# Performance work log

Measured on AMD Instinct MI355X. Metric: run time of the kernel, lower is better.

The kernel has to match this reference:

```python
import jax, jax.numpy as jnp
import numpy as np
from jax import lax

B, T, F, D, K = 64, 1000, 140, 256, 7
TAU, V_TH, EPS, ALPHA = 2.0, 1.0, 1e-5, 2.0
PAD = (K - 1) // 2

# Heaviside spike with ATan surrogate gradient (spikingjelly default, alpha=2)
@jax.custom_vjp
def spike_fn(x):
    return (x >= 0.0).astype(x.dtype)

def _spike_fwd(x):
    return spike_fn(x), x

def _spike_bwd(x, g):
    sg = (ALPHA / 2.0) / (1.0 + (jnp.pi / 2.0 * ALPHA * x) ** 2)
    return (g * sg,)

spike_fn.defvjp(_spike_fwd, _spike_bwd)

def lif(x_seq):
    """Multi-step LIF: v += (x - v)/tau, hard reset to 0 on spike. x_seq: (T,B,D)."""
    def step(v, x):
        v = v + (x - v) / TAU
        s = spike_fn(v - V_TH)
        return v * (1.0 - s), s
    _, spikes = lax.scan(step, jnp.zeros_like(x_seq[0]), x_seq)
    return spikes

def bn(x, g, b, m, v):
    # eval-mode BatchNorm1d over channel dim D (last axis of (T,B,D))
    return (x - m) * (g * lax.rsqrt(v + EPS)) + b

def setup_inputs() -> dict:
    key = jax.random.key(0)
    ks = jax.random.split(key, 4)
    s = 0.05
    return {
        "x": jax.random.normal(ks[0], (B, T, F), jnp.float32),
        "pw_w": jax.random.normal(ks[1], (D, F), jnp.float32) * s,
        "pw_b": jnp.zeros((D,), jnp.float32),
        "dw_w": jax.random.normal(ks[2], (D, 1, K), jnp.float32) * s,  # depthwise (O,I/g,K)
        "bn1_g": jnp.ones((D,), jnp.float32),
        "bn1_b": jnp.zeros((D,), jnp.float32),
        "bn1_m": jnp.zeros((D,), jnp.float32),
        "bn1_v": jnp.ones((D,), jnp.float32),
        "lin_w": jax.random.normal(ks[3], (D, D), jnp.float32) * s,
        "bn2_g": jnp.ones((D,), jnp.float32),
        "bn2_b": jnp.zeros((D,), jnp.float32),
        "bn2_m": jnp.zeros((D,), jnp.float32),
        "bn2_v": jnp.ones((D,), jnp.float32),
    }

def reference(x, pw_w, pw_b, dw_w, bn1_g, bn1_b, bn1_m, bn1_v,
              lin_w, bn2_g, bn2_b, bn2_m, bn2_v):
    # pointwise conv: (B,T,F) -> (B,D,T)
    h = jnp.einsum('btf,df->bdt', x, pw_w) + pw_b[None, :, None]
    # depthwise temporal conv, groups=D, same padding
    h = lax.conv_general_dilated(h, dw_w, window_strides=(1,),
                                 padding=[(PAD, PAD)], feature_group_count=D,
                                 dimension_numbers=('NCH', 'OIH', 'NCH'))
    h = jnp.transpose(h, (2, 0, 1))  # (T,B,D) multi-step layout
    h = lif(bn(h, bn1_g, bn1_b, bn1_m, bn1_v))
    residual = h
    h = jnp.einsum('tbd,ed->tbe', h, lin_w)
    h = lif(bn(h, bn2_g, bn2_b, bn2_m, bn2_v))
    return h + residual
```

## Files before the change

### kernel.cpp

```cpp
#include <hip/hip_runtime.h>
#include <hip/hip_bf16.h>

#define B_  64
#define T_  1000
#define F_  140
#define D_  256
#define EPS_ 1e-5f

#define CL_ 50
#define NC_ 20
#define W_  24

#define CW2_ 96
#define NCH_ 11
#define HST_ 132

typedef __attribute__((ext_vector_type(8))) short bf16x8;
typedef __attribute__((ext_vector_type(4))) float f32x4;
typedef unsigned long long u64;

static __device__ inline short f2bf(float f) {
  __hip_bfloat16 h = __float2bfloat16(f);
  return *reinterpret_cast<short*>(&h);
}
static __device__ inline float bf2f(short s) {
  unsigned int u = ((unsigned int)(unsigned short)s) << 16;
  return __uint_as_float(u);
}

__global__ __launch_bounds__(256) void k0_prep(const float* __restrict__ lw,
                                               float* __restrict__ lwT,
                                               const float* __restrict__ pw,
                                               short* __restrict__ wbf) {
  int i = blockIdx.x * 256 + threadIdx.x;
  if (i < 65536) {
    int e = i >> 8, d = i & 255;
    lwT[(size_t)d * D_ + e] = lw[(size_t)e * D_ + d];
  } else if (i < 65536 + 256 * 160) {
    int j = i - 65536;
    int n = j / 160, k = j - n * 160;
    wbf[j] = (k < F_) ? f2bf(pw[(size_t)n * F_ + k]) : (short)0;
  }
}

__global__ __launch_bounds__(256) void k12_fused(const float* __restrict__ x,
                                                 const short* __restrict__ wbf,
                                                 const float* __restrict__ bias,
                                                 const float* __restrict__ dww,
                                                 const float* __restrict__ g1,
                                                 const float* __restrict__ b1,
                                                 const float* __restrict__ m1,
                                                 const float* __restrict__ v1,
                                                 u64* __restrict__ bits) {
  __shared__ short smem[20480];
  short* As = smem;
  short* Bs = smem + 10240;
  const int b = blockIdx.x;
  const int c = blockIdx.y;
  const int half = blockIdx.z;
  const int n0g = half * 128;
  const int tb = CW2_ * c - 27;
  const int tid = threadIdx.x;
  const int lane = tid & 63, wv = tid >> 6;
  const int lr = lane & 15, quad = lane >> 4;
  const int mr = (wv & 1) * 64, nc0 = (wv >> 1) * 64;

  const int srow = tid >> 1;
  const int kh = (tid & 1) * 16;
  const int ta = tb + srow;
  const bool arow_ok = (ta >= 0) && (ta < T_);
  const float* xrow = x + ((size_t)b * T_ + ta) * F_;
  const short* wrow = wbf + (size_t)(n0g + srow) * 160 + kh;

  auto stage = [&](int kc, int buf) {
    short tmp[16];
#pragma unroll
    for (int q = 0; q < 4; q++) {
      int kg = kc + kh + q * 4;
      float4 av = make_float4(0.f, 0.f, 0.f, 0.f);
      if (arow_ok && kg < F_) av = *(const float4*)(xrow + kg);
      tmp[q * 4 + 0] = f2bf(av.x); tmp[q * 4 + 1] = f2bf(av.y);
      tmp[q * 4 + 2] = f2bf(av.z); tmp[q * 4 + 3] = f2bf(av.w);
    }
    short* ap = As + buf * 5120 + srow * 40 + kh;
    *(bf16x8*)(ap + 0) = *(bf16x8*)(tmp + 0);
    *(bf16x8*)(ap + 8) = *(bf16x8*)(tmp + 8);
    short* bp = Bs + buf * 5120 + srow * 40 + kh;
    *(bf16x8*)(bp + 0) = *(const bf16x8*)(wrow + kc + 0);
    *(bf16x8*)(bp + 8) = *(const bf16x8*)(wrow + kc + 8);
  };

  f32x4 acc[4][4] = {};
  stage(0, 0);
  __syncthreads();
#pragma unroll
  for (int kk = 0; kk < 5; kk++) {
    const int cur = kk & 1;
    if (kk < 4) stage((kk + 1) * 32, cur ^ 1);
    const short* ap = As + cur * 5120 + quad * 8;
    const short* bp = Bs + cur * 5120 + quad * 8;
    bf16x8 af[4], bfr[4];
#pragma unroll
    for (int i = 0; i < 4; i++) af[i] = *(const bf16x8*)(ap + (mr + i * 16 + lr) * 40);
#pragma unroll
    for (int j = 0; j < 4; j++) bfr[j] = *(const bf16x8*)(bp + (nc0 + j * 16 + lr) * 40);
#pragma unroll
    for (int i = 0; i < 4; i++)
#pragma unroll
      for (int j = 0; j < 4; j++)
        acc[i][j] = __builtin_amdgcn_mfma_f32_16x16x32_bf16(af[i], bfr[j], acc[i][j], 0, 0, 0);
    __syncthreads();
  }

  short* hbuf = smem;
#pragma unroll
  for (int j = 0; j < 4; j++) {
    const int n = nc0 + j * 16 + lr;
    const float badd = bias[n0g + n];
#pragma unroll
    for (int i = 0; i < 4; i++) {
      const int m = mr + i * 16 + quad * 4;
#pragma unroll
      for (int r = 0; r < 4; r++) {
        const int t = tb + m + r;
        short val = (t >= 0 && t < T_) ? f2bf(acc[i][j][r] + badd) : (short)0;
        hbuf[(m + r) * HST_ + n] = val;
      }
    }
  }
  __syncthreads();

  if (tid < 128) {
    const int d = n0g + tid;
    const float scv = g1[d] * rsqrtf(v1[d] + EPS_);
    float w2[7];
#pragma unroll
    for (int k = 0; k < 7; k++) w2[k] = dww[d * 7 + k] * (0.5f * scv);
    const float sh2 = 0.5f * (b1[d] - m1[d] * scv);

    const int wb = (c == 0) ? 24 : 0;
    float win0 = bf2f(hbuf[(wb + 0) * HST_ + tid]);
    float win1 = bf2f(hbuf[(wb + 1) * HST_ + tid]);
    float win2 = bf2f(hbuf[(wb + 2) * HST_ + tid]);
    float win3 = bf2f(hbuf[(wb + 3) * HST_ + tid]);
    float win4 = bf2f(hbuf[(wb + 4) * HST_ + tid]);
    float win5 = bf2f(hbuf[(wb + 5) * HST_ + tid]);
    float v = 0.f;

    if (c != 0) {
#pragma unroll
      for (int s0 = 0; s0 < 24; s0 += 8) {
        float tap[8];
#pragma unroll
        for (int g = 0; g < 8; g++) tap[g] = bf2f(hbuf[(s0 + g + 6) * HST_ + tid]);
#pragma unroll
        for (int g = 0; g < 8; g++) {
          float u2 = win0 * w2[0] + win1 * w2[1] + win2 * w2[2] + win3 * w2[3] +
                     win4 * w2[4] + win5 * w2[5] + tap[g] * w2[6] + sh2;
          v = 0.5f * v + u2;
          v = (v >= 1.0f) ? 0.f : v;
          win0 = win1; win1 = win2; win2 = win3; win3 = win4; win4 = win5; win5 = tap[g];
        }
      }
    }
    const int tw0 = CW2_ * c;
    const int dq = half * 2 + (tid >> 6);
    u64* bp2 = bits + ((size_t)b * T_ + tw0) * 4 + dq;
    const bool lane0 = ((tid & 63) == 0);
    const int smax = T_ - tw0;
#pragma unroll
    for (int s0 = 0; s0 < 96; s0 += 8) {
      float tap[8];
#pragma unroll
      for (int g = 0; g < 8; g++) tap[g] = bf2f(hbuf[(s0 + g + 30) * HST_ + tid]);
#pragma unroll
      for (int g = 0; g < 8; g++) {
        float u2 = win0 * w2[0] + win1 * w2[1] + win2 * w2[2] + win3 * w2[3] +
                   win4 * w2[4] + win5 * w2[5] + tap[g] * w2[6] + sh2;
        v = 0.5f * v + u2;
        bool sp = (v >= 1.0f);
        u64 mask = __ballot(sp);
        if (lane0 && (s0 + g) < smax) bp2[(size_t)(s0 + g) * 4] = mask;
        v = sp ? 0.f : v;
        win0 = win1; win1 = win2; win2 = win3; win3 = win4; win4 = win5; win5 = tap[g];
      }
    }
  }
}

__global__ __launch_bounds__(256) void k3_lin_lif(const u64* __restrict__ bits,
                                                  const float* __restrict__ lwT,
                                                  const float* __restrict__ g2,
                                                  const float* __restrict__ b2,
                                                  const float* __restrict__ m2,
                                                  const float* __restrict__ v2,
                                                  float* __restrict__ out) {
  __shared__ u64 sb[(CL_ + W_) * 4];
  const int b = blockIdx.x;
  const int t0 = blockIdx.y * CL_;
  const int tstart = (t0 >= W_) ? t0 - W_ : 0;
  const int nwarm = t0 - tstart;
  const int nsteps = nwarm + CL_;
  const int e = threadIdx.x;
  const u64* gbp = bits + ((size_t)b * T_ + tstart) * 4;
  for (int i = e; i < nsteps * 4; i += 256) sb[i] = gbp[i];
  __syncthreads();

  const float sc = g2[e] * rsqrtf(v2[e] + EPS_);
  const float shf = b2[e] - m2[e] * sc;
  const int eq = e >> 6, eb = e & 63;
  float v = 0.f;

  if (nwarm) {
#pragma unroll
    for (int s0 = 0; s0 < 24; s0 += 4) {
      u64 a0[4], a1[4], a2[4], a3[4];
#pragma unroll
      for (int g = 0; g < 4; g++) {
        a0[g] = sb[(s0 + g) * 4 + 0]; a1[g] = sb[(s0 + g) * 4 + 1];
        a2[g] = sb[(s0 + g) * 4 + 2]; a3[g] = sb[(s0 + g) * 4 + 3];
      }
#pragma unroll
      for (int g = 0; g < 4; g++) {
        float u = shf;
        if (a0[g] | a1[g] | a2[g] | a3[g]) {
          float acc = 0.f;
          u64 mm;
          mm = a0[g]; while (mm) { int l = __builtin_ctzll(mm); mm &= mm - 1; acc += lwT[(size_t)(l) * D_ + e]; }
          mm = a1[g]; while (mm) { int l = __builtin_ctzll(mm); mm &= mm - 1; acc += lwT[(size_t)(64 + l) * D_ + e]; }
          mm = a2[g]; while (mm) { int l = __builtin_ctzll(mm); mm &= mm - 1; acc += lwT[(size_t)(128 + l) * D_ + e]; }
          mm = a3[g]; while (mm) { int l = __builtin_ctzll(mm); mm &= mm - 1; acc += lwT[(size_t)(192 + l) * D_ + e]; }
          u = acc * sc + shf;
        }
        v = 0.5f * (v + u);
        v = (v >= 1.0f) ? 0.f : v;
      }
    }
  }
  float* op = out + ((size_t)t0 * B_ + b) * D_ + e;
  const size_t ts = (size_t)B_ * D_;
#pragma unroll
  for (int s0 = 0; s0 < 50; s0 += 5) {
    u64 a0[5], a1[5], a2[5], a3[5];
#pragma unroll
    for (int g = 0; g < 5; g++) {
      const int s = nwarm + s0 + g;
      a0[g] = sb[s * 4 + 0]; a1[g] = sb[s * 4 + 1];
      a2[g] = sb[s * 4 + 2]; a3[g] = sb[s * 4 + 3];
    }
#pragma unroll
    for (int g = 0; g < 5; g++) {
      float u = shf;
      if (a0[g] | a1[g] | a2[g] | a3[g]) {
        float acc = 0.f;
        u64 mm;
        mm = a0[g]; while (mm) { int l = __builtin_ctzll(mm); mm &= mm - 1; acc += lwT[(size_t)(l) * D_ + e]; }
        mm = a1[g]; while (mm) { int l = __builtin_ctzll(mm); mm &= mm - 1; acc += lwT[(size_t)(64 + l) * D_ + e]; }
        mm = a2[g]; while (mm) { int l = __builtin_ctzll(mm); mm &= mm - 1; acc += lwT[(size_t)(128 + l) * D_ + e]; }
        mm = a3[g]; while (mm) { int l = __builtin_ctzll(mm); mm &= mm - 1; acc += lwT[(size_t)(192 + l) * D_ + e]; }
        u = acc * sc + shf;
      }
      v = 0.5f * (v + u);
      bool sp = (v >= 1.0f);
      u64 myw = (eq == 0) ? a0[g] : (eq == 1) ? a1[g] : (eq == 2) ? a2[g] : a3[g];
      float s1 = (float)((myw >> eb) & 1ull);
      op[(size_t)(s0 + g) * ts] = (sp ? 1.0f : 0.0f) + s1;
      v = sp ? 0.f : v;
    }
  }
}

extern "C" void kernel_launch(void* const* d_in, const int* in_sizes, int n_in,
                              void* d_out, int out_size, void* d_ws, size_t ws_size,
                              hipStream_t stream) {
  const float* x    = (const float*)d_in[0];
  const float* pw_w = (const float*)d_in[1];
  const float* pw_b = (const float*)d_in[2];
  const float* dw_w = (const float*)d_in[3];
  const float* g1   = (const float*)d_in[4];
  const float* b1   = (const float*)d_in[5];
  const float* m1   = (const float*)d_in[6];
  const float* v1   = (const float*)d_in[7];
  const float* lw   = (const float*)d_in[8];
  const float* g2   = (const float*)d_in[9];
  const float* b2   = (const float*)d_in[10];
  const float* m2   = (const float*)d_in[11];
  const float* v2   = (const float*)d_in[12];
  float* out = (float*)d_out;

  char* ws = (char*)d_ws;
  u64* bits = (u64*)ws;
  float* lwT = (float*)(ws + 2048000);
  short* wbf = (short*)(ws + 2048000 + 262144);

  k0_prep<<<(65536 + 256 * 160 + 255) / 256, 256, 0, stream>>>(lw, lwT, pw_w, wbf);
  dim3 g_k12(B_, NCH_, 2);
  k12_fused<<<g_k12, 256, 0, stream>>>(x, wbf, pw_b, dw_w, g1, b1, m1, v1, bits);
  dim3 g_k3(B_, NC_);
  k3_lin_lif<<<g_k3, 256, 0, stream>>>(bits, lwT, g2, b2, m2, v2, out);
}
```

Baseline: 176.9 us.

## Restructure fused conv-LIF kernel into short 34-step chunks covering all channels

The fused pointwise-conv plus depthwise-conv plus LIF kernel now gives each block all 256 channels and a 34-step time window instead of half the channels over 96 steps. This makes the grid 64x30 rather than 64x11x2, so all 256 threads take part in the serial LIF scan and each thread's sequential chain is shorter. The pointwise weights are pre-swizzled into MFMA fragment order and loaded straight from global memory, and the whole A tile is staged once instead of double-buffered. In exchange, the 27-step warm-up recompute is a much larger share of each chunk, and the larger LDS footprint may lower occupancy.

```diff
diff --git a/kernel.cpp b/kernel.cpp
--- a/kernel.cpp
+++ b/kernel.cpp
@@ -11,11 +11,13 @@
 #define NC_ 20
 #define W_  24
 
-#define CW2_ 96
-#define NCH_ 11
-#define HST_ 132
+#define CW3_ 34
+#define NCH3_ 30
+#define HST3_ 268
+#define AST_ 168
 
 typedef __attribute__((ext_vector_type(8))) short bf16x8;
+typedef __attribute__((ext_vector_type(4))) short bf16x4;
 typedef __attribute__((ext_vector_type(4))) float f32x4;
 typedef unsigned long long u64;
 
@@ -31,20 +33,25 @@
 __global__ __launch_bounds__(256) void k0_prep(const float* __restrict__ lw,
                                                float* __restrict__ lwT,
                                                const float* __restrict__ pw,
-                                               short* __restrict__ wbf) {
+                                               short* __restrict__ wfrag) {
   int i = blockIdx.x * 256 + threadIdx.x;
   if (i < 65536) {
     int e = i >> 8, d = i & 255;
     lwT[(size_t)d * D_ + e] = lw[(size_t)e * D_ + d];
-  } else if (i < 65536 + 256 * 160) {
+  } else if (i < 65536 + 40960) {
     int j = i - 65536;
-    int n = j / 160, k = j - n * 160;
-    wbf[j] = (k < F_) ? f2bf(pw[(size_t)n * F_ + k]) : (short)0;
+    int q = j & 7;
+    int lane = (j >> 3) & 63;
+    int rest = j >> 9;
+    int kk = rest % 5, ntile = rest / 5;
+    int n = ntile * 16 + (lane & 15);
+    int k = kk * 32 + (lane >> 4) * 8 + q;
+    wfrag[j] = (k < F_) ? f2bf(pw[(size_t)n * F_ + k]) : (short)0;
   }
 }
 
 __global__ __launch_bounds__(256) void k12_fused(const float* __restrict__ x,
-                                                 const short* __restrict__ wbf,
+                                                 const short* __restrict__ wfrag,
                                                  const float* __restrict__ bias,
                                                  const float* __restrict__ dww,
                                                  const float* __restrict__ g1,
@@ -52,86 +59,84 @@
                                                  const float* __restrict__ m1,
                                                  const float* __restrict__ v1,
                                                  u64* __restrict__ bits) {
-  __shared__ short smem[20480];
-  short* As = smem;
-  short* Bs = smem + 10240;
+  __shared__ short smem[64 * HST3_];
+  short* Abuf = smem;
+  short* hbuf = smem;
   const int b = blockIdx.x;
   const int c = blockIdx.y;
-  const int half = blockIdx.z;
-  const int n0g = half * 128;
-  const int tb = CW2_ * c - 27;
+  const int tb = CW3_ * c - 27;
   const int tid = threadIdx.x;
   const int lane = tid & 63, wv = tid >> 6;
   const int lr = lane & 15, quad = lane >> 4;
-  const int mr = (wv & 1) * 64, nc0 = (wv >> 1) * 64;
-
-  const int srow = tid >> 1;
-  const int kh = (tid & 1) * 16;
-  const int ta = tb + srow;
-  const bool arow_ok = (ta >= 0) && (ta < T_);
-  const float* xrow = x + ((size_t)b * T_ + ta) * F_;
-  const short* wrow = wbf + (size_t)(n0g + srow) * 160 + kh;
-
-  auto stage = [&](int kc, int buf) {
-    short tmp[16];
-#pragma unroll
-    for (int q = 0; q < 4; q++) {
-      int kg = kc + kh + q * 4;
-      float4 av = make_float4(0.f, 0.f, 0.f, 0.f);
-      if (arow_ok && kg < F_) av = *(const float4*)(xrow + kg);
-      tmp[q * 4 + 0] = f2bf(av.x); tmp[q * 4 + 1] = f2bf(av.y);
-      tmp[q * 4 + 2] = f2bf(av.z); tmp[q * 4 + 3] = f2bf(av.w);
-    }
-    short* ap = As + buf * 5120 + srow * 40 + kh;
-    *(bf16x8*)(ap + 0) = *(bf16x8*)(tmp + 0);
-    *(bf16x8*)(ap + 8) = *(bf16x8*)(tmp + 8);
-    short* bp = Bs + buf * 5120 + srow * 40 + kh;
-    *(bf16x8*)(bp + 0) = *(const bf16x8*)(wrow + kc + 0);
-    *(bf16x8*)(bp + 8) = *(const bf16x8*)(wrow + kc + 8);
-  };
+
+  {
+    const int arow = tid >> 2, aseg = tid & 3;
+    const int ak0 = aseg * 36;
+    const int anum4 = (aseg == 3) ? 8 : 9;
+    const int ta = tb + arow;
+    short* adst = Abuf + arow * AST_ + ak0;
+    if (ta >= 0 && ta < T_) {
+      const float* xrow = x + ((size_t)b * T_ + ta) * F_ + ak0;
+#pragma unroll
+      for (int q = 0; q < 9; q++) {
+        if (q < anum4) {
+          float4 av = *(const float4*)(xrow + q * 4);
+          bf16x4 pk = {f2bf(av.x), f2bf(av.y), f2bf(av.z), f2bf(av.w)};
+          *(bf16x4*)(adst + q * 4) = pk;
+        }
+      }
+    } else {
+      bf16x4 z = {0, 0, 0, 0};
+#pragma unroll
+      for (int q = 0; q < 9; q++)
+        if (q < anum4) *(bf16x4*)(adst + q * 4) = z;
+    }
+    if (aseg == 3) {
+      bf16x4 z = {0, 0, 0, 0};
+#pragma unroll
+      for (int q = 0; q < 5; q++) *(bf16x4*)(adst + 32 + q * 4) = z;
+    }
+  }
+  __syncthreads();
 
   f32x4 acc[4][4] = {};
-  stage(0, 0);
-  __syncthreads();
+  const short* wfb = wfrag + (size_t)(wv * 4 * 5) * 512 + lane * 8;
 #pragma unroll
   for (int kk = 0; kk < 5; kk++) {
-    const int cur = kk & 1;
-    if (kk < 4) stage((kk + 1) * 32, cur ^ 1);
-    const short* ap = As + cur * 5120 + quad * 8;
-    const short* bp = Bs + cur * 5120 + quad * 8;
-    bf16x8 af[4], bfr[4];
-#pragma unroll
-    for (int i = 0; i < 4; i++) af[i] = *(const bf16x8*)(ap + (mr + i * 16 + lr) * 40);
-#pragma unroll
-    for (int j = 0; j < 4; j++) bfr[j] = *(const bf16x8*)(bp + (nc0 + j * 16 + lr) * 40);
+    bf16x8 bfr[4], af[4];
+#pragma unroll
+    for (int j = 0; j < 4; j++)
+      bfr[j] = *(const bf16x8*)(wfb + (size_t)(j * 5 + kk) * 512);
+#pragma unroll
+    for (int i = 0; i < 4; i++)
+      af[i] = *(const bf16x8*)(Abuf + (i * 16 + lr) * AST_ + kk * 32 + quad * 8);
 #pragma unroll
     for (int i = 0; i < 4; i++)
 #pragma unroll
       for (int j = 0; j < 4; j++)
         acc[i][j] = __builtin_amdgcn_mfma_f32_16x16x32_bf16(af[i], bfr[j], acc[i][j], 0, 0, 0);
-    __syncthreads();
-  }
-
-  short* hbuf = smem;
+  }
+  __syncthreads();
+
 #pragma unroll
   for (int j = 0; j < 4; j++) {
-    const int n = nc0 + j * 16 + lr;
-    const float badd = bias[n0g + n];
+    const int n = wv * 64 + j * 16 + lr;
+    const float badd = bias[n];
 #pragma unroll
     for (int i = 0; i < 4; i++) {
-      const int m = mr + i * 16 + quad * 4;
 #pragma unroll
       for (int r = 0; r < 4; r++) {
-        const int t = tb + m + r;
+        const int row = i * 16 + quad * 4 + r;
+        const int t = tb + row;
         short val = (t >= 0 && t < T_) ? f2bf(acc[i][j][r] + badd) : (short)0;
-        hbuf[(m + r) * HST_ + n] = val;
+        hbuf[row * HST3_ + n] = val;
       }
     }
   }
   __syncthreads();
 
-  if (tid < 128) {
-    const int d = n0g + tid;
+  {
+    const int d = tid;
     const float scv = g1[d] * rsqrtf(v1[d] + EPS_);
     float w2[7];
 #pragma unroll
@@ -139,12 +144,12 @@
     const float sh2 = 0.5f * (b1[d] - m1[d] * scv);
 
     const int wb = (c == 0) ? 24 : 0;
-    float win0 = bf2f(hbuf[(wb + 0) * HST_ + tid]);
-    float win1 = bf2f(hbuf[(wb + 1) * HST_ + tid]);
-    float win2 = bf2f(hbuf[(wb + 2) * HST_ + tid]);
-    float win3 = bf2f(hbuf[(wb + 3) * HST_ + tid]);
-    float win4 = bf2f(hbuf[(wb + 4) * HST_ + tid]);
-    float win5 = bf2f(hbuf[(wb + 5) * HST_ + tid]);
+    float win0 = bf2f(hbuf[(wb + 0) * HST3_ + d]);
+    float win1 = bf2f(hbuf[(wb + 1) * HST3_ + d]);
+    float win2 = bf2f(hbuf[(wb + 2) * HST3_ + d]);
+    float win3 = bf2f(hbuf[(wb + 3) * HST3_ + d]);
+    float win4 = bf2f(hbuf[(wb + 4) * HST3_ + d]);
+    float win5 = bf2f(hbuf[(wb + 5) * HST3_ + d]);
     float v = 0.f;
 
     if (c != 0) {
@@ -152,7 +157,7 @@
       for (int s0 = 0; s0 < 24; s0 += 8) {
         float tap[8];
 #pragma unroll
-        for (int g = 0; g < 8; g++) tap[g] = bf2f(hbuf[(s0 + g + 6) * HST_ + tid]);
+        for (int g = 0; g < 8; g++) tap[g] = bf2f(hbuf[(s0 + g + 6) * HST3_ + d]);
 #pragma unroll
         for (int g = 0; g < 8; g++) {
           float u2 = win0 * w2[0] + win1 * w2[1] + win2 * w2[2] + win3 * w2[3] +
@@ -163,16 +168,15 @@
         }
       }
     }
-    const int tw0 = CW2_ * c;
-    const int dq = half * 2 + (tid >> 6);
-    u64* bp2 = bits + ((size_t)b * T_ + tw0) * 4 + dq;
-    const bool lane0 = ((tid & 63) == 0);
+    const int tw0 = CW3_ * c;
     const int smax = T_ - tw0;
-#pragma unroll
-    for (int s0 = 0; s0 < 96; s0 += 8) {
+    u64* bp = bits + ((size_t)b * T_ + tw0) * 4 + wv;
+    const bool lane0 = (lane == 0);
+#pragma unroll
+    for (int s0 = 0; s0 < 32; s0 += 8) {
       float tap[8];
 #pragma unroll
-      for (int g = 0; g < 8; g++) tap[g] = bf2f(hbuf[(s0 + g + 30) * HST_ + tid]);
+      for (int g = 0; g < 8; g++) tap[g] = bf2f(hbuf[(s0 + g + 30) * HST3_ + d]);
 #pragma unroll
       for (int g = 0; g < 8; g++) {
         float u2 = win0 * w2[0] + win1 * w2[1] + win2 * w2[2] + win3 * w2[3] +
@@ -180,7 +184,23 @@
         v = 0.5f * v + u2;
         bool sp = (v >= 1.0f);
         u64 mask = __ballot(sp);
-        if (lane0 && (s0 + g) < smax) bp2[(size_t)(s0 + g) * 4] = mask;
+        if (lane0 && (s0 + g) < smax) bp[(size_t)(s0 + g) * 4] = mask;
+        v = sp ? 0.f : v;
+        win0 = win1; win1 = win2; win2 = win3; win3 = win4; win4 = win5; win5 = tap[g];
+      }
+    }
+    {
+      float tap[2];
+#pragma unroll
+      for (int g = 0; g < 2; g++) tap[g] = bf2f(hbuf[(32 + g + 30) * HST3_ + d]);
+#pragma unroll
+      for (int g = 0; g < 2; g++) {
+        float u2 = win0 * w2[0] + win1 * w2[1] + win2 * w2[2] + win3 * w2[3] +
+                   win4 * w2[4] + win5 * w2[5] + tap[g] * w2[6] + sh2;
+        v = 0.5f * v + u2;
+        bool sp = (v >= 1.0f);
+        u64 mask = __ballot(sp);
+        if (lane0 && (32 + g) < smax) bp[(size_t)(32 + g) * 4] = mask;
         v = sp ? 0.f : v;
         win0 = win1; win1 = win2; win2 = win3; win3 = win4; win4 = win5; win5 = tap[g];
       }
@@ -291,11 +311,11 @@
   char* ws = (char*)d_ws;
   u64* bits = (u64*)ws;
   float* lwT = (float*)(ws + 2048000);
-  short* wbf = (short*)(ws + 2048000 + 262144);
-
-  k0_prep<<<(65536 + 256 * 160 + 255) / 256, 256, 0, stream>>>(lw, lwT, pw_w, wbf);
-  dim3 g_k12(B_, NCH_, 2);
-  k12_fused<<<g_k12, 256, 0, stream>>>(x, wbf, pw_b, dw_w, g1, b1, m1, v1, bits);
+  short* wfrag = (short*)(ws + 2048000 + 262144);
+
+  k0_prep<<<(65536 + 40960 + 255) / 256, 256, 0, stream>>>(lw, lwT, pw_w, wfrag);
+  dim3 g_k12(B_, NCH3_);
+  k12_fused<<<g_k12, 256, 0, stream>>>(x, wfrag, pw_b, dw_w, g1, b1, m1, v1, bits);
   dim3 g_k3(B_, NC_);
   k3_lin_lif<<<g_k3, 256, 0, stream>>>(bits, lwT, g2, b2, m2, v2, out);
 }
```

New measurement: 160.4 us. -9.3%, faster.
